# Performance work log

Hardware: AMD Instinct MI355X
Metric: run time of the kernel (lower is better)

## Reference

```python
import jax, jax.numpy as jnp
import numpy as np

D_MODEL = 1024
N_HEADS = 16
HEAD_DIM = D_MODEL // N_HEADS
D_FF = 4096
LN_EPS = 1e-5


def _layer_norm(x, gamma, beta):
    mu = jnp.mean(x, axis=-1, keepdims=True)
    var = jnp.var(x, axis=-1, keepdims=True)
    return (x - mu) * jax.lax.rsqrt(var + LN_EPS) * gamma + beta


def setup_inputs() -> dict:
    key = jax.random.key(0)
    ks = jax.random.split(key, 16)
    s = 1.0 / np.sqrt(D_MODEL)
    sf = 1.0 / np.sqrt(D_FF)
    return {
        "x": jax.random.normal(ks[0], (4, 2048, D_MODEL), dtype=jnp.float32),
        "w_q": jax.random.uniform(ks[1], (D_MODEL, D_MODEL), jnp.float32, -s, s),
        "b_q": jax.random.uniform(ks[2], (D_MODEL,), jnp.float32, -s, s),
        "w_k": jax.random.uniform(ks[3], (D_MODEL, D_MODEL), jnp.float32, -s, s),
        "b_k": jax.random.uniform(ks[4], (D_MODEL,), jnp.float32, -s, s),
        "w_v": jax.random.uniform(ks[5], (D_MODEL, D_MODEL), jnp.float32, -s, s),
        "b_v": jax.random.uniform(ks[6], (D_MODEL,), jnp.float32, -s, s),
        "w_o": jax.random.uniform(ks[7], (D_MODEL, D_MODEL), jnp.float32, -s, s),
        "b_o": jax.random.uniform(ks[8], (D_MODEL,), jnp.float32, -s, s),
        "ln1_g": jnp.ones((D_MODEL,), jnp.float32),
        "ln1_b": jnp.zeros((D_MODEL,), jnp.float32),
        "w1": jax.random.uniform(ks[9], (D_MODEL, D_FF), jnp.float32, -s, s),
        "b1": jax.random.uniform(ks[10], (D_FF,), jnp.float32, -s, s),
        "w2": jax.random.uniform(ks[11], (D_FF, D_MODEL), jnp.float32, -sf, sf),
        "b2": jax.random.uniform(ks[12], (D_MODEL,), jnp.float32, -sf, sf),
        "ln2_g": jnp.ones((D_MODEL,), jnp.float32),
        "ln2_b": jnp.zeros((D_MODEL,), jnp.float32),
    }


def reference(x, w_q, b_q, w_k, b_k, w_v, b_v, w_o, b_o,
              ln1_g, ln1_b, w1, b1, w2, b2, ln2_g, ln2_b):
    B, S, D = x.shape
    # projections -> [B, H, S, Hd]
    def split_heads(t):
        return t.reshape(B, S, N_HEADS, HEAD_DIM).transpose(0, 2, 1, 3)
    q = split_heads(x @ w_q + b_q)
    k = split_heads(x @ w_k + b_k)
    v = split_heads(x @ w_v + b_v)
    scale = jnp.float32(np.sqrt(HEAD_DIM))
    scores = jnp.einsum('bhqd,bhkd->bhqk', q, k) / scale
    attn = jax.nn.softmax(scores, axis=-1)  # dropout = identity in eval
    ctx = jnp.einsum('bhqk,bhkd->bhqd', attn, v)
    ctx = ctx.transpose(0, 2, 1, 3).reshape(B, S, D)
    attn_out = ctx @ w_o + b_o
    h = _layer_norm(x + attn_out, ln1_g, ln1_b)
    ffn = jax.nn.relu(h @ w1 + b1) @ w2 + b2
    return _layer_norm(h + ffn, ln2_g, ln2_b)
```

## Files before the change

### kernel.cpp

```cpp
#include <hip/hip_runtime.h>
#include <cstdint>
#include <cstddef>

typedef unsigned short u16;
typedef short s16x8 __attribute__((ext_vector_type(8)));
typedef unsigned short u16x8 __attribute__((ext_vector_type(8)));
typedef unsigned short u16x4 __attribute__((ext_vector_type(4)));
typedef float f32x4 __attribute__((ext_vector_type(4)));

#define MFMA_BF16(a, b, c) __builtin_amdgcn_mfma_f32_16x16x32_bf16((a), (b), (c), 0, 0, 0)

__device__ __forceinline__ float b2f(u16 u) {
    union { unsigned int i; float f; } x;
    x.i = ((unsigned int)u) << 16;
    return x.f;
}
__device__ __forceinline__ u16 f2b(float f) {
    union { float f; unsigned int i; } x;
    x.f = f;
    return (u16)((x.i + 0x8000u) >> 16);
}
__device__ __forceinline__ float exp2_hw(float x) {
    float r;
    asm volatile("v_exp_f32 %0, %1" : "=v"(r) : "v"(x));
    return r;
}

__device__ __forceinline__ void gload_lds16(const u16* g, u16* l) {
    __builtin_amdgcn_global_load_lds((__attribute__((address_space(1))) void*)(g),
                                     (__attribute__((address_space(3))) void*)(l),
                                     16, 0, 0);
}

__global__ __launch_bounds__(256)
void cvt_f32_bf16(const float* __restrict__ in, u16* __restrict__ out) {
    const int i = (blockIdx.x * 256 + threadIdx.x) * 8;
    float4 a = *(const float4*)(in + i);
    float4 b = *(const float4*)(in + i + 4);
    u16x8 o;
    o[0] = f2b(a.x); o[1] = f2b(a.y); o[2] = f2b(a.z); o[3] = f2b(a.w);
    o[4] = f2b(b.x); o[5] = f2b(b.y); o[6] = f2b(b.z); o[7] = f2b(b.w);
    *(u16x8*)(out + i) = o;
}

__global__ __launch_bounds__(256)
void transpose_cvt(const float* __restrict__ in, u16* __restrict__ out, int R, int C) {
    __shared__ u16 t[64][68];
    const int tc = blockIdx.x * 64, tr = blockIdx.y * 64;
    for (int i = 0; i < 16; i++) {
        int idx = threadIdx.x + i * 256;
        int r = idx >> 6, c = idx & 63;
        t[r][c] = f2b(in[(size_t)(tr + r) * C + tc + c]);
    }
    __syncthreads();
    for (int i = 0; i < 16; i++) {
        int idx = threadIdx.x + i * 256;
        int r = idx >> 6, c = idx & 63;
        out[(size_t)(tc + r) * R + tr + c] = t[c][r];
    }
}

enum { EPI_PLAIN = 0, EPI_RELU = 1, EPI_QKV = 2 };
#define SC_QK 0.1803368801111204f

template <int EPI>
__global__ __launch_bounds__(256)
void gemm_bt(const u16* __restrict__ A, const u16* __restrict__ Bt,
             const float* __restrict__ bias0, const float* __restrict__ bias1,
             const float* __restrict__ bias2,
             u16* __restrict__ C0, u16* __restrict__ C1, u16* __restrict__ C2,
             int M, int N, int K) {
    __shared__ u16 As[128 * 64];
    __shared__ u16 Bs[128 * 64];
    const int tid = threadIdx.x;
    const int lane = tid & 63;
    const int wave = tid >> 6;
    const int qd = lane >> 4, cl = lane & 15;
    const int wr = (wave >> 1) * 64, wc = (wave & 1) * 64;
    const int m0 = blockIdx.x * 128, n0 = blockIdx.y * 128;

    const u16* AgP[4];
    const u16* BgP[4];
    int dsto[4];
    for (int c = 0; c < 4; c++) {
        const int d = tid * 8 + c * 2048;
        const int row = d >> 6;
        const int sblk = ((d >> 3) & 7) ^ (row & 7);
        AgP[c] = A + (size_t)(m0 + row) * K + sblk * 8;
        BgP[c] = Bt + (size_t)(n0 + row) * K + sblk * 8;
        dsto[c] = d;
    }

    const f32x4 Z = {0.f, 0.f, 0.f, 0.f};
    f32x4 acc[4][4];
    for (int i = 0; i < 4; i++)
        for (int j = 0; j < 4; j++) acc[i][j] = Z;

    for (int k = 0; k < K; k += 64) {
        __syncthreads();
        for (int c = 0; c < 4; c++) {
            gload_lds16(AgP[c] + k, As + dsto[c]);
            gload_lds16(BgP[c] + k, Bs + dsto[c]);
        }
        __syncthreads();
        for (int kk = 0; kk < 2; kk++) {
            s16x8 af[4], bfr[4];
            for (int i = 0; i < 4; i++) {
                const int row = wr + i * 16 + cl;
                af[i] = *(const s16x8*)(As + row * 64 +
                                        (((kk << 2) | qd) ^ (row & 7)) * 8);
            }
            for (int j = 0; j < 4; j++) {
                const int row = wc + j * 16 + cl;
                bfr[j] = *(const s16x8*)(Bs + row * 64 +
                                         (((kk << 2) | qd) ^ (row & 7)) * 8);
            }
            for (int i = 0; i < 4; i++)
                for (int j = 0; j < 4; j++)
                    acc[i][j] = MFMA_BF16(af[i], bfr[j], acc[i][j]);
        }
    }

    for (int j = 0; j < 4; j++) {
        const int col = n0 + wc + j * 16 + cl;
        float bv;
        if (EPI == EPI_QKV) {
            const int t = col >> 10, nn = col & 1023;
            const float* bp = (t == 0) ? bias0 : ((t == 1) ? bias1 : bias2);
            bv = bp[nn];
        } else {
            bv = bias0[col];
        }
        if (EPI == EPI_QKV && (col >> 10) == 2) {
            const int nn = col & 1023;
            const int hh = nn >> 6, d = nn & 63;
            for (int i = 0; i < 4; i++) {
                const int row0 = m0 + wr + i * 16 + qd * 4;
                const int b = row0 >> 11, s = row0 & 2047;
                const int bh = b * 16 + hh;
                u16x4 pk;
                for (int r = 0; r < 4; r++) pk[r] = f2b(acc[i][j][r] + bv);
                *(u16x4*)(&C2[((size_t)bh * 64 + d) * 2048 + s]) = pk;
            }
        } else {
            for (int i = 0; i < 4; i++) {
                for (int r = 0; r < 4; r++) {
                    const int row = m0 + wr + i * 16 + qd * 4 + r;
                    float v = acc[i][j][r] + bv;
                    if (EPI == EPI_RELU) v = fmaxf(v, 0.f);
                    if (EPI == EPI_QKV) {
                        const int t = col >> 10, nn = col & 1023;
                        const int hh = nn >> 6, d = nn & 63;
                        const int b = row >> 11, s = row & 2047;
                        const int bh = b * 16 + hh;
                        if (t == 0)
                            C0[((size_t)bh * 2048 + s) * 64 + d] = f2b(v * SC_QK);
                        else
                            C1[((size_t)bh * 2048 + s) * 64 + d] = f2b(v);
                    } else {
                        C0[(size_t)row * N + col] = f2b(v);
                    }
                }
            }
        }
    }
}

__global__ __launch_bounds__(256)
void flash_attn(const u16* __restrict__ Q, const u16* __restrict__ K,
                const u16* __restrict__ Vt, u16* __restrict__ ctx) {
    __shared__ u16 Ks[64 * 64];
    __shared__ u16 Vs[64 * 64];
    __shared__ u16 Ps[4][32 * 72];
    const int tid = threadIdx.x, lane = tid & 63, wave = tid >> 6;
    const int qd = lane >> 4, cl = lane & 15;
    const int bh = blockIdx.y;
    const int s0 = blockIdx.x * 128 + wave * 32;

    const u16* Qb = Q + ((size_t)bh * 2048 + s0) * 64;
    s16x8 qf[2][2];
    for (int m = 0; m < 2; m++) {
        qf[m][0] = *(const s16x8*)(Qb + (m * 16 + cl) * 64 + qd * 8);
        qf[m][1] = *(const s16x8*)(Qb + (m * 16 + cl) * 64 + 32 + qd * 8);
    }

    const f32x4 Z = {0.f, 0.f, 0.f, 0.f};
    f32x4 o_acc[2][4], l_lane[2];
    for (int m = 0; m < 2; m++) {
        l_lane[m] = Z;
        for (int t = 0; t < 4; t++) o_acc[m][t] = Z;
    }

    const u16* Kb = K + (size_t)bh * 2048 * 64;
    const u16* Vb = Vt + (size_t)bh * 64 * 2048;

    const int e0 = tid, e1 = tid + 256;
    const int r0 = e0 >> 3, bb0 = (e0 & 7) ^ (r0 & 7);
    const int r1 = e1 >> 3, bb1 = (e1 & 7) ^ (r1 & 7);
    u16* pw = &Ps[wave][0];

    for (int kb = 0; kb < 32; kb++) {
        __syncthreads();
        gload_lds16(Kb + (size_t)(kb * 64 + r0) * 64 + bb0 * 8, Ks + e0 * 8);
        gload_lds16(Kb + (size_t)(kb * 64 + r1) * 64 + bb1 * 8, Ks + e1 * 8);
        gload_lds16(Vb + (size_t)r0 * 2048 + kb * 64 + bb0 * 8, Vs + e0 * 8);
        gload_lds16(Vb + (size_t)r1 * 2048 + kb * 64 + bb1 * 8, Vs + e1 * 8);
        __syncthreads();

        f32x4 sacc[2][4];
        for (int m = 0; m < 2; m++)
            for (int t = 0; t < 4; t++) sacc[m][t] = Z;
        for (int t = 0; t < 4; t++) {
            const int row = t * 16 + cl;
            s16x8 kf0 = *(const s16x8*)(Ks + row * 64 + (qd ^ (row & 7)) * 8);
            s16x8 kf1 = *(const s16x8*)(Ks + row * 64 + ((qd + 4) ^ (row & 7)) * 8);
            for (int m = 0; m < 2; m++) {
                sacc[m][t] = MFMA_BF16(qf[m][0], kf0, sacc[m][t]);
                sacc[m][t] = MFMA_BF16(qf[m][1], kf1, sacc[m][t]);
            }
        }

        for (int m = 0; m < 2; m++)
            for (int t = 0; t < 4; t++) {
                f32x4 p;
                for (int r = 0; r < 4; r++) p[r] = exp2_hw(sacc[m][t][r]);
                l_lane[m] += p;
                for (int r = 0; r < 4; r++)
                    pw[(m * 16 + qd * 4 + r) * 72 + t * 16 + cl] = f2b(p[r]);
            }

        for (int kk = 0; kk < 2; kk++) {
            s16x8 vf[4];
            for (int t = 0; t < 4; t++) {
                const int row = t * 16 + cl;
                vf[t] = *(const s16x8*)(Vs + row * 64 +
                                        ((kk * 4 + qd) ^ (row & 7)) * 8);
            }
            for (int m = 0; m < 2; m++) {
                s16x8 pf = *(const s16x8*)(pw + (m * 16 + cl) * 72 + kk * 32 + qd * 8);
                for (int t = 0; t < 4; t++)
                    o_acc[m][t] = MFMA_BF16(pf, vf[t], o_acc[m][t]);
            }
        }
    }

    const int b = bh >> 4, hh = bh & 15;
    for (int m = 0; m < 2; m++)
        for (int r = 0; r < 4; r++) {
            float l = l_lane[m][r];
            for (int off = 1; off < 16; off <<= 1)
                l += __shfl_xor(l, off, 16);
            const float inv = 1.f / l;
            const int s = s0 + m * 16 + qd * 4 + r;
            for (int t = 0; t < 4; t++)
                ctx[((size_t)(b * 2048 + s)) * 1024 + hh * 64 + t * 16 + cl] =
                    f2b(o_acc[m][t][r] * inv);
        }
}

template <int MODE>
__global__ __launch_bounds__(256)
void ln_res(const void* __restrict__ Xv, const u16* __restrict__ Y,
            const float* __restrict__ G, const float* __restrict__ Bp,
            void* __restrict__ Ov) {
    const int row = blockIdx.x * 4 + (threadIdx.x >> 6);
    const int lane = threadIdx.x & 63;
    const int off = lane * 16;
    float v[16];
    float s = 0.f, s2 = 0.f;
    const u16* y = Y + (size_t)row * 1024 + off;
    if (MODE == 0) {
        const float* X = (const float*)Xv + (size_t)row * 1024 + off;
        for (int i = 0; i < 2; i++) {
            float4 xa = *(const float4*)(X + i * 8);
            float4 xb = *(const float4*)(X + i * 8 + 4);
            u16x8 yv = *(const u16x8*)(y + i * 8);
            float xs[8] = {xa.x, xa.y, xa.z, xa.w, xb.x, xb.y, xb.z, xb.w};
            for (int j = 0; j < 8; j++) {
                const float t = xs[j] + b2f(yv[j]);
                v[i * 8 + j] = t;
                s += t;
                s2 += t * t;
            }
        }
    } else {
        const u16* X = (const u16*)Xv + (size_t)row * 1024 + off;
        for (int i = 0; i < 2; i++) {
            u16x8 xv = *(const u16x8*)(X + i * 8);
            u16x8 yv = *(const u16x8*)(y + i * 8);
            for (int j = 0; j < 8; j++) {
                const float t = b2f(xv[j]) + b2f(yv[j]);
                v[i * 8 + j] = t;
                s += t;
                s2 += t * t;
            }
        }
    }
    for (int o = 32; o >= 1; o >>= 1) {
        s += __shfl_xor(s, o, 64);
        s2 += __shfl_xor(s2, o, 64);
    }
    const float mu = s * (1.f / 1024.f);
    const float var = s2 * (1.f / 1024.f) - mu * mu;
    const float rs = rsqrtf(var + 1e-5f);
    const float* g = G + off;
    const float* bp = Bp + off;
    for (int i = 0; i < 2; i++) {
        float4 ga = *(const float4*)(g + i * 8);
        float4 gb = *(const float4*)(g + i * 8 + 4);
        float4 ba = *(const float4*)(bp + i * 8);
        float4 bb = *(const float4*)(bp + i * 8 + 4);
        float gs[8] = {ga.x, ga.y, ga.z, ga.w, gb.x, gb.y, gb.z, gb.w};
        float bs[8] = {ba.x, ba.y, ba.z, ba.w, bb.x, bb.y, bb.z, bb.w};
        if (MODE == 0) {
            u16* o = (u16*)Ov + (size_t)row * 1024 + off;
            u16x8 ov;
            for (int j = 0; j < 8; j++)
                ov[j] = f2b((v[i * 8 + j] - mu) * rs * gs[j] + bs[j]);
            *(u16x8*)(o + i * 8) = ov;
        } else {
            float* o = (float*)Ov + (size_t)row * 1024 + off;
            float4 o0, o1;
            o0.x = (v[i * 8 + 0] - mu) * rs * gs[0] + bs[0];
            o0.y = (v[i * 8 + 1] - mu) * rs * gs[1] + bs[1];
            o0.z = (v[i * 8 + 2] - mu) * rs * gs[2] + bs[2];
            o0.w = (v[i * 8 + 3] - mu) * rs * gs[3] + bs[3];
            o1.x = (v[i * 8 + 4] - mu) * rs * gs[4] + bs[4];
            o1.y = (v[i * 8 + 5] - mu) * rs * gs[5] + bs[5];
            o1.z = (v[i * 8 + 6] - mu) * rs * gs[6] + bs[6];
            o1.w = (v[i * 8 + 7] - mu) * rs * gs[7] + bs[7];
            *(float4*)(o + i * 8) = o0;
            *(float4*)(o + i * 8 + 4) = o1;
        }
    }
}

extern "C" void kernel_launch(void* const* d_in, const int* in_sizes, int n_in,
                              void* d_out, int out_size, void* d_ws, size_t ws_size,
                              hipStream_t stream) {
    const float* x    = (const float*)d_in[0];
    const float* w_q  = (const float*)d_in[1];
    const float* b_q  = (const float*)d_in[2];
    const float* w_k  = (const float*)d_in[3];
    const float* b_k  = (const float*)d_in[4];
    const float* w_v  = (const float*)d_in[5];
    const float* b_v  = (const float*)d_in[6];
    const float* w_o  = (const float*)d_in[7];
    const float* b_o  = (const float*)d_in[8];
    const float* ln1g = (const float*)d_in[9];
    const float* ln1b = (const float*)d_in[10];
    const float* w1   = (const float*)d_in[11];
    const float* b1   = (const float*)d_in[12];
    const float* w2   = (const float*)d_in[13];
    const float* b2   = (const float*)d_in[14];
    const float* ln2g = (const float*)d_in[15];
    const float* ln2b = (const float*)d_in[16];
    float* out = (float*)d_out;

    char* ws = (char*)d_ws;
    const size_t MB = 1024 * 1024;
    u16* wqkv_t = (u16*)(ws + 0);
    u16* wo_t   = (u16*)(ws + 6 * MB);
    u16* w1_t   = (u16*)(ws + 8 * MB);
    u16* w2_t   = (u16*)(ws + 16 * MB);
    u16* x_bf   = (u16*)(ws + 24 * MB);
    u16* Qs     = (u16*)(ws + 40 * MB);
    u16* Kk     = (u16*)(ws + 56 * MB);
    u16* Vt     = (u16*)(ws + 72 * MB);
    u16* ctx    = (u16*)(ws + 88 * MB);
    u16* attn   = (u16*)(ws + 104 * MB);
    u16* h      = attn;
    u16* ffn1   = (u16*)(ws + 24 * MB);
    u16* ffn2   = (u16*)(ws + 88 * MB);

    transpose_cvt<<<dim3(16, 16), 256, 0, stream>>>(w_q, wqkv_t, 1024, 1024);
    transpose_cvt<<<dim3(16, 16), 256, 0, stream>>>(w_k, wqkv_t + 1024 * 1024, 1024, 1024);
    transpose_cvt<<<dim3(16, 16), 256, 0, stream>>>(w_v, wqkv_t + 2 * 1024 * 1024, 1024, 1024);
    transpose_cvt<<<dim3(16, 16), 256, 0, stream>>>(w_o, wo_t, 1024, 1024);
    transpose_cvt<<<dim3(64, 16), 256, 0, stream>>>(w1, w1_t, 1024, 4096);
    transpose_cvt<<<dim3(16, 64), 256, 0, stream>>>(w2, w2_t, 4096, 1024);

    cvt_f32_bf16<<<4096, 256, 0, stream>>>(x, x_bf);

    gemm_bt<EPI_QKV><<<dim3(64, 24), 256, 0, stream>>>(
        x_bf, wqkv_t, b_q, b_k, b_v, Qs, Kk, Vt, 8192, 3072, 1024);

    flash_attn<<<dim3(16, 64), 256, 0, stream>>>(Qs, Kk, Vt, ctx);

    gemm_bt<EPI_PLAIN><<<dim3(64, 8), 256, 0, stream>>>(
        ctx, wo_t, b_o, nullptr, nullptr, attn, nullptr, nullptr, 8192, 1024, 1024);

    ln_res<0><<<2048, 256, 0, stream>>>(x, attn, ln1g, ln1b, h);

    gemm_bt<EPI_RELU><<<dim3(64, 32), 256, 0, stream>>>(
        h, w1_t, b1, nullptr, nullptr, ffn1, nullptr, nullptr, 8192, 4096, 1024);
    gemm_bt<EPI_PLAIN><<<dim3(64, 8), 256, 0, stream>>>(
        ffn1, w2_t, b2, nullptr, nullptr, ffn2, nullptr, nullptr, 8192, 1024, 4096);

    ln_res<1><<<2048, 256, 0, stream>>>(h, ffn2, ln2g, ln2b, out);

    (void)in_sizes; (void)n_in; (void)out_size; (void)ws_size;
}
```

Measured before the change: 534.0 us.

## Merge weight prep into one launch, add GEMM occupancy hint, reorder attention grid

Replaces six transpose launches and the input conversion with a single prep_all kernel that dispatches on block index, removing launch overhead and serialization between the small prep kernels. It also adds a min-blocks-per-CU hint of 3 to the GEMM launch bounds, which may cap register use and raise occupancy. It swaps the flash-attention grid so batch-head runs along x and sequence tiles along y, which changes the block scheduling order and may alter K/V cache reuse. The register cap could cause spills in the GEMM.

```diff
diff --git a/kernel.cpp b/kernel.cpp
--- a/kernel.cpp
+++ b/kernel.cpp
@@ -32,21 +32,11 @@
                                      16, 0, 0);
 }
 
-__global__ __launch_bounds__(256)
-void cvt_f32_bf16(const float* __restrict__ in, u16* __restrict__ out) {
-    const int i = (blockIdx.x * 256 + threadIdx.x) * 8;
-    float4 a = *(const float4*)(in + i);
-    float4 b = *(const float4*)(in + i + 4);
-    u16x8 o;
-    o[0] = f2b(a.x); o[1] = f2b(a.y); o[2] = f2b(a.z); o[3] = f2b(a.w);
-    o[4] = f2b(b.x); o[5] = f2b(b.y); o[6] = f2b(b.z); o[7] = f2b(b.w);
-    *(u16x8*)(out + i) = o;
-}
-
-__global__ __launch_bounds__(256)
-void transpose_cvt(const float* __restrict__ in, u16* __restrict__ out, int R, int C) {
+__device__ __forceinline__ void transpose_tile(const float* __restrict__ in,
+                                               u16* __restrict__ out,
+                                               int R, int C, int bx, int by) {
     __shared__ u16 t[64][68];
-    const int tc = blockIdx.x * 64, tr = blockIdx.y * 64;
+    const int tc = bx * 64, tr = by * 64;
     for (int i = 0; i < 16; i++) {
         int idx = threadIdx.x + i * 256;
         int r = idx >> 6, c = idx & 63;
@@ -60,11 +50,45 @@
     }
 }
 
+__global__ __launch_bounds__(256)
+void prep_all(const float* __restrict__ w_q, const float* __restrict__ w_k,
+              const float* __restrict__ w_v, const float* __restrict__ w_o,
+              const float* __restrict__ w1, const float* __restrict__ w2,
+              const float* __restrict__ x,
+              u16* __restrict__ wqkv_t, u16* __restrict__ wo_t,
+              u16* __restrict__ w1_t, u16* __restrict__ w2_t,
+              u16* __restrict__ x_bf) {
+    const int id = blockIdx.x;
+    if (id < 1024) {
+        const int j = id >> 8, lid = id & 255;
+        const float* in = (j == 0) ? w_q : (j == 1) ? w_k : (j == 2) ? w_v : w_o;
+        u16* out = (j == 0) ? wqkv_t
+                 : (j == 1) ? wqkv_t + 1024 * 1024
+                 : (j == 2) ? wqkv_t + 2 * 1024 * 1024
+                 : wo_t;
+        transpose_tile(in, out, 1024, 1024, lid & 15, lid >> 4);
+    } else if (id < 2048) {
+        const int lid = id - 1024;
+        transpose_tile(w1, w1_t, 1024, 4096, lid & 63, lid >> 6);
+    } else if (id < 3072) {
+        const int lid = id - 2048;
+        transpose_tile(w2, w2_t, 4096, 1024, lid & 15, lid >> 4);
+    } else {
+        const int i = ((id - 3072) * 256 + threadIdx.x) * 8;
+        float4 a = *(const float4*)(x + i);
+        float4 b = *(const float4*)(x + i + 4);
+        u16x8 o;
+        o[0] = f2b(a.x); o[1] = f2b(a.y); o[2] = f2b(a.z); o[3] = f2b(a.w);
+        o[4] = f2b(b.x); o[5] = f2b(b.y); o[6] = f2b(b.z); o[7] = f2b(b.w);
+        *(u16x8*)(x_bf + i) = o;
+    }
+}
+
 enum { EPI_PLAIN = 0, EPI_RELU = 1, EPI_QKV = 2 };
 #define SC_QK 0.1803368801111204f
 
 template <int EPI>
-__global__ __launch_bounds__(256)
+__global__ __launch_bounds__(256, 3)
 void gemm_bt(const u16* __restrict__ A, const u16* __restrict__ Bt,
              const float* __restrict__ bias0, const float* __restrict__ bias1,
              const float* __restrict__ bias2,
@@ -174,8 +198,8 @@
     __shared__ u16 Ps[4][32 * 72];
     const int tid = threadIdx.x, lane = tid & 63, wave = tid >> 6;
     const int qd = lane >> 4, cl = lane & 15;
-    const int bh = blockIdx.y;
-    const int s0 = blockIdx.x * 128 + wave * 32;
+    const int bh = blockIdx.x;
+    const int s0 = blockIdx.y * 128 + wave * 32;
 
     const u16* Qb = Q + ((size_t)bh * 2048 + s0) * 64;
     s16x8 qf[2][2];
@@ -373,19 +397,13 @@
     u16* ffn1   = (u16*)(ws + 24 * MB);
     u16* ffn2   = (u16*)(ws + 88 * MB);
 
-    transpose_cvt<<<dim3(16, 16), 256, 0, stream>>>(w_q, wqkv_t, 1024, 1024);
-    transpose_cvt<<<dim3(16, 16), 256, 0, stream>>>(w_k, wqkv_t + 1024 * 1024, 1024, 1024);
-    transpose_cvt<<<dim3(16, 16), 256, 0, stream>>>(w_v, wqkv_t + 2 * 1024 * 1024, 1024, 1024);
-    transpose_cvt<<<dim3(16, 16), 256, 0, stream>>>(w_o, wo_t, 1024, 1024);
-    transpose_cvt<<<dim3(64, 16), 256, 0, stream>>>(w1, w1_t, 1024, 4096);
-    transpose_cvt<<<dim3(16, 64), 256, 0, stream>>>(w2, w2_t, 4096, 1024);
-
-    cvt_f32_bf16<<<4096, 256, 0, stream>>>(x, x_bf);
+    prep_all<<<7168, 256, 0, stream>>>(w_q, w_k, w_v, w_o, w1, w2, x,
+                                       wqkv_t, wo_t, w1_t, w2_t, x_bf);
 
     gemm_bt<EPI_QKV><<<dim3(64, 24), 256, 0, stream>>>(
         x_bf, wqkv_t, b_q, b_k, b_v, Qs, Kk, Vt, 8192, 3072, 1024);
 
-    flash_attn<<<dim3(16, 64), 256, 0, stream>>>(Qs, Kk, Vt, ctx);
+    flash_attn<<<dim3(64, 16), 256, 0, stream>>>(Qs, Kk, Vt, ctx);
 
     gemm_bt<EPI_PLAIN><<<dim3(64, 8), 256, 0, stream>>>(
         ctx, wo_t, b_o, nullptr, nullptr, attn, nullptr, nullptr, 8192, 1024, 1024);
```

New measurement: 484.2 us. 9.3% less time.
